# Kernel optimization log

Measured on AMD Instinct MI355X. Metric: run time of the kernel, lower is better.

## Reference

```python
import jax, jax.numpy as jnp
import numpy as np

PATCH = 16
B, C, H, W = 4, 3, 512, 512
N = 4096  # patches per image


def setup_inputs() -> dict:
    key = jax.random.key(0)
    k1, k2, k3, k4 = jax.random.split(key, 4)
    fuse = jax.random.normal(k1, (B, C, H, W), jnp.float32)
    img1 = jax.random.normal(k2, (B, C, H, W), jnp.float32)
    img2 = jax.random.normal(k3, (B, C, H, W), jnp.float32)
    # valid top-left (h, w) so h+PATCH <= H, w+PATCH <= W
    coords = jax.random.randint(k4, (B, N, 2), 0, H - PATCH + 1, dtype=jnp.int32)
    return {"fuse": fuse, "img1": img1, "img2": img2, "coords": coords}


def _extract_patches(image, coords):
    # image: [B,C,H,W], coords: [B,N,2] -> patches [B,C,N,P] with P=PATCH*PATCH
    c = image.shape[1]

    def one(img_b, hw):
        p = jax.lax.dynamic_slice(img_b, (0, hw[0], hw[1]), (c, PATCH, PATCH))
        return p.reshape(c, PATCH * PATCH)

    pat = jax.vmap(jax.vmap(one, in_axes=(None, 0)), in_axes=(0, 0))(image, coords)  # [B,N,C,P]
    return jnp.transpose(pat, (0, 2, 1, 3))  # [B,C,N,P]


def reference(fuse, img1, img2, coords):
    pf = _extract_patches(fuse, coords)
    p1 = _extract_patches(img1, coords)
    p2 = _extract_patches(img2, coords)
    mu1 = jnp.mean(p1, axis=-1, keepdims=True)
    mu2 = jnp.mean(p2, axis=-1, keepdims=True)
    sd1 = jnp.sqrt(jnp.mean((p1 - mu1) ** 2, axis=-1, keepdims=True))
    sd2 = jnp.sqrt(jnp.mean((p2 - mu2) ** 2, axis=-1, keepdims=True))
    denom = sd1 + sd2 + 1e-6
    target = (sd1 / denom) * p1 + (sd2 / denom) * p2
    return jnp.mean(jnp.abs(pf - target))
```

## Files before the change

kernel.cpp:

```cpp
#include <hip/hip_runtime.h>

#define BD 4
#define CD 3
#define HD 512
#define WD 512
#define NPAT 4096
#define NP (BD * NPAT)
#define PLANE (HD * WD)
#define PPW 2
#define PPB (PPW * 4)
#define NBLK (NP / PPB)
#define TOTAL_ELEMS (4.0 * 3.0 * 4096.0 * 256.0)

typedef float f4 __attribute__((ext_vector_type(4), aligned(4)));

template <int CTRL>
__device__ __forceinline__ float dpp_add(float x) {
    int y = __builtin_amdgcn_update_dpp(0, __float_as_int(x), CTRL, 0xF, 0xF, true);
    return x + __int_as_float(y);
}

__device__ __forceinline__ float wave_sum64(float x) {
    x = dpp_add<0xB1>(x);
    x = dpp_add<0x4E>(x);
    x = dpp_add<0x124>(x);
    x = dpp_add<0x128>(x);
    x += __shfl_xor(x, 16, 64);
    x += __shfl_xor(x, 32, 64);
    return x;
}

__global__ __launch_bounds__(256) void build_order(
    const int* __restrict__ coords, unsigned int* __restrict__ order)
{
    __shared__ unsigned short cnt[256][18];
    __shared__ unsigned short part[16][17];
    __shared__ unsigned int   base[16];

    const int t = threadIdx.x;
    const int b = blockIdx.x;
    const int key16 = t >> 4;
    const int sub   = t & 15;

    #pragma unroll
    for (int k = 0; k < 16; ++k) cnt[t][k] = 0;
    __syncthreads();

    const int2* c2 = (const int2*)coords;
    unsigned int pk[16];
    #pragma unroll
    for (int i = 0; i < 16; ++i) {
        const int p = (b << 12) + (i << 8) + t;
        const int2 hw = c2[p];
        pk[i] = ((unsigned)b << 18) | ((unsigned)hw.x << 9) | (unsigned)hw.y;
        cnt[t][hw.x >> 5]++;
    }
    __syncthreads();

    unsigned run = 0;
    #pragma unroll
    for (int tt = sub * 16; tt < sub * 16 + 16; ++tt) run += cnt[tt][key16];
    part[key16][sub] = (unsigned short)run;
    __syncthreads();

    if (t < 16) {
        unsigned r = 0;
        #pragma unroll
        for (int s = 0; s < 16; ++s) { unsigned v = part[t][s]; part[t][s] = (unsigned short)r; r += v; }
        base[t] = r;
    }
    __syncthreads();
    if (t == 0) {
        unsigned r = 0;
        #pragma unroll
        for (int k = 0; k < 16; ++k) { unsigned v = base[k]; base[k] = r; r += v; }
    }
    __syncthreads();

    {
        unsigned r = part[key16][sub];
        #pragma unroll
        for (int tt = sub * 16; tt < sub * 16 + 16; ++tt) {
            unsigned v = cnt[tt][key16]; cnt[tt][key16] = (unsigned short)r; r += v;
        }
    }
    __syncthreads();

    #pragma unroll
    for (int i = 0; i < 16; ++i) {
        const unsigned key = (pk[i] >> 14) & 15;
        const unsigned pos = base[key] + cnt[t][key];
        cnt[t][key]++;
        order[(b << 12) + pos] = pk[i];
    }
}

__global__ __launch_bounds__(256) void patch_stage1(
    const float* __restrict__ fuse,
    const float* __restrict__ img1,
    const float* __restrict__ img2,
    const unsigned int* __restrict__ order,
    float* __restrict__ partials)
{
    const int lane = threadIdx.x & 63;
    const int wave = threadIdx.x >> 6;
    const int bid  = blockIdx.x;
    const int slot0 = (((bid & 7) * (NBLK / 8) + (bid >> 3)) << 3) + wave * PPW;

    const uint2 ord = *(const uint2*)(order + slot0);

    const int wA = ord.x & 511, hA = (ord.x >> 9) & 511, bA = ord.x >> 18;
    const int wB = ord.y & 511, hB = (ord.y >> 9) & 511, bB = ord.y >> 18;

    const int roff = (lane >> 2) * WD + (lane & 3) * 4;
    const size_t baseA = ((size_t)(bA * CD) * HD + hA) * WD + wA + roff;
    const size_t baseB = ((size_t)(bB * CD) * HD + hB) * WD + wB + roff;

    f4 vfA[3], v1A[3], v2A[3], vfB[3], v1B[3], v2B[3];
    #pragma unroll
    for (int c = 0; c < CD; ++c) {
        vfA[c] = *(const f4*)(fuse + baseA + (size_t)c * PLANE);
        v1A[c] = *(const f4*)(img1 + baseA + (size_t)c * PLANE);
        v2A[c] = *(const f4*)(img2 + baseA + (size_t)c * PLANE);
        vfB[c] = *(const f4*)(fuse + baseB + (size_t)c * PLANE);
        v1B[c] = *(const f4*)(img1 + baseB + (size_t)c * PLANE);
        v2B[c] = *(const f4*)(img2 + baseB + (size_t)c * PLANE);
    }

    float s1[2][3], q1[2][3], s2[2][3], q2[2][3];
    #pragma unroll
    for (int c = 0; c < CD; ++c) {
        s1[0][c] = v1A[c].x + v1A[c].y + v1A[c].z + v1A[c].w;
        q1[0][c] = v1A[c].x*v1A[c].x + v1A[c].y*v1A[c].y + v1A[c].z*v1A[c].z + v1A[c].w*v1A[c].w;
        s2[0][c] = v2A[c].x + v2A[c].y + v2A[c].z + v2A[c].w;
        q2[0][c] = v2A[c].x*v2A[c].x + v2A[c].y*v2A[c].y + v2A[c].z*v2A[c].z + v2A[c].w*v2A[c].w;
        s1[1][c] = v1B[c].x + v1B[c].y + v1B[c].z + v1B[c].w;
        q1[1][c] = v1B[c].x*v1B[c].x + v1B[c].y*v1B[c].y + v1B[c].z*v1B[c].z + v1B[c].w*v1B[c].w;
        s2[1][c] = v2B[c].x + v2B[c].y + v2B[c].z + v2B[c].w;
        q2[1][c] = v2B[c].x*v2B[c].x + v2B[c].y*v2B[c].y + v2B[c].z*v2B[c].z + v2B[c].w*v2B[c].w;
    }

    #pragma unroll
    for (int u = 0; u < 2; ++u) {
        #pragma unroll
        for (int c = 0; c < CD; ++c) {
            s1[u][c] = wave_sum64(s1[u][c]);
            q1[u][c] = wave_sum64(q1[u][c]);
            s2[u][c] = wave_sum64(s2[u][c]);
            q2[u][c] = wave_sum64(q2[u][c]);
        }
    }

    const float inv = 1.f / 256.f;
    float acc = 0.f;
    #pragma unroll
    for (int u = 0; u < 2; ++u) {
        #pragma unroll
        for (int c = 0; c < CD; ++c) {
            const float mu1 = s1[u][c] * inv;
            const float mu2 = s2[u][c] * inv;
            const float sd1 = sqrtf(fmaxf(q1[u][c] * inv - mu1 * mu1, 0.f));
            const float sd2 = sqrtf(fmaxf(q2[u][c] * inv - mu2 * mu2, 0.f));
            const float denom = sd1 + sd2 + 1e-6f;
            const float w1 = sd1 / denom;
            const float w2 = sd2 / denom;
            const f4 vf = u ? vfB[c] : vfA[c];
            const f4 v1 = u ? v1B[c] : v1A[c];
            const f4 v2 = u ? v2B[c] : v2A[c];
            acc += fabsf(vf.x - (w1 * v1.x + w2 * v2.x))
                 + fabsf(vf.y - (w1 * v1.y + w2 * v2.y))
                 + fabsf(vf.z - (w1 * v1.z + w2 * v2.z))
                 + fabsf(vf.w - (w1 * v1.w + w2 * v2.w));
        }
    }

    acc = wave_sum64(acc);

    __shared__ float partsm[4];
    if (lane == 0) partsm[wave] = acc;
    __syncthreads();
    if (threadIdx.x == 0)
        partials[bid] = partsm[0] + partsm[1] + partsm[2] + partsm[3];
}

__global__ __launch_bounds__(256) void patch_stage2(
    const float* __restrict__ partials, float* __restrict__ out)
{
    float s = 0.f;
    for (int i = threadIdx.x; i < NBLK; i += 256)
        s += partials[i];

    s = wave_sum64(s);

    __shared__ float partsm[4];
    const int lane = threadIdx.x & 63;
    const int wave = threadIdx.x >> 6;
    if (lane == 0) partsm[wave] = s;
    __syncthreads();
    if (threadIdx.x == 0)
        out[0] = (partsm[0] + partsm[1] + partsm[2] + partsm[3]) * (float)(1.0 / TOTAL_ELEMS);
}

extern "C" void kernel_launch(void* const* d_in, const int* in_sizes, int n_in,
                              void* d_out, int out_size, void* d_ws, size_t ws_size,
                              hipStream_t stream) {
    const float* fuse   = (const float*)d_in[0];
    const float* img1   = (const float*)d_in[1];
    const float* img2   = (const float*)d_in[2];
    const int*   coords = (const int*)d_in[3];
    float* out = (float*)d_out;

    unsigned int* order    = (unsigned int*)d_ws;
    float*        partials = (float*)((char*)d_ws + NP * 4);

    build_order<<<BD, 256, 0, stream>>>(coords, order);
    patch_stage1<<<NBLK, 256, 0, stream>>>(fuse, img1, img2, order, partials);
    patch_stage2<<<1, 256, 0, stream>>>(partials, out);
}
```

Before: 30.73 us.

## Sort patches by 2D 32x32 tile buckets instead of row bands

The counting-sort key in build_order changes from 16 row bands to 256 spatial tiles (h/32, w/32). The goal is to make consecutive stage1 blocks read spatially nearby patches and improve L2/cache reuse. To support the larger key space, build_order now uses byte counters in a large padded LDS array, a per-thread serial column scan, and a wave shuffle prefix scan. In exchange, the sort kernel uses much more shared memory and does a longer serial scan.

```diff
diff --git a/kernel.cpp b/kernel.cpp
--- a/kernel.cpp
+++ b/kernel.cpp
@@ -11,6 +11,7 @@
 #define PPB (PPW * 4)
 #define NBLK (NP / PPB)
 #define TOTAL_ELEMS (4.0 * 3.0 * 4096.0 * 256.0)
+#define CSTRIDE 260
 
 typedef float f4 __attribute__((ext_vector_type(4), aligned(4)));
 
@@ -33,64 +34,67 @@
 __global__ __launch_bounds__(256) void build_order(
     const int* __restrict__ coords, unsigned int* __restrict__ order)
 {
-    __shared__ unsigned short cnt[256][18];
-    __shared__ unsigned short part[16][17];
-    __shared__ unsigned int   base[16];
+    __shared__ unsigned char  cnt[256 * CSTRIDE];
+    __shared__ unsigned short total[256];
+    __shared__ unsigned int   base[256];
 
     const int t = threadIdx.x;
     const int b = blockIdx.x;
-    const int key16 = t >> 4;
-    const int sub   = t & 15;
-
-    #pragma unroll
-    for (int k = 0; k < 16; ++k) cnt[t][k] = 0;
+
+    {
+        unsigned int* row = (unsigned int*)(cnt + t * CSTRIDE);
+        #pragma unroll
+        for (int k = 0; k < CSTRIDE / 4; ++k) row[k] = 0u;
+    }
     __syncthreads();
 
     const int2* c2 = (const int2*)coords;
-    unsigned int pk[16];
+    unsigned int  pk[16];
+    unsigned char kk[16];
     #pragma unroll
     for (int i = 0; i < 16; ++i) {
         const int p = (b << 12) + (i << 8) + t;
         const int2 hw = c2[p];
         pk[i] = ((unsigned)b << 18) | ((unsigned)hw.x << 9) | (unsigned)hw.y;
-        cnt[t][hw.x >> 5]++;
-    }
-    __syncthreads();
-
-    unsigned run = 0;
-    #pragma unroll
-    for (int tt = sub * 16; tt < sub * 16 + 16; ++tt) run += cnt[tt][key16];
-    part[key16][sub] = (unsigned short)run;
-    __syncthreads();
-
-    if (t < 16) {
-        unsigned r = 0;
-        #pragma unroll
-        for (int s = 0; s < 16; ++s) { unsigned v = part[t][s]; part[t][s] = (unsigned short)r; r += v; }
-        base[t] = r;
-    }
-    __syncthreads();
-    if (t == 0) {
-        unsigned r = 0;
-        #pragma unroll
-        for (int k = 0; k < 16; ++k) { unsigned v = base[k]; base[k] = r; r += v; }
+        kk[i] = (unsigned char)(((hw.x >> 5) << 4) | (hw.y >> 5));
+        cnt[t * CSTRIDE + kk[i]]++;
     }
     __syncthreads();
 
     {
-        unsigned r = part[key16][sub];
-        #pragma unroll
-        for (int tt = sub * 16; tt < sub * 16 + 16; ++tt) {
-            unsigned v = cnt[tt][key16]; cnt[tt][key16] = (unsigned short)r; r += v;
-        }
+        unsigned int run = 0;
+        for (int tt = 0; tt < 256; ++tt) {
+            const unsigned int v = cnt[tt * CSTRIDE + t];
+            cnt[tt * CSTRIDE + t] = (unsigned char)run;
+            run += v;
+        }
+        total[t] = (unsigned short)run;
+    }
+    __syncthreads();
+
+    if (t < 64) {
+        const unsigned int t0 = total[4 * t],     t1 = total[4 * t + 1];
+        const unsigned int t2 = total[4 * t + 2], t3 = total[4 * t + 3];
+        const unsigned int lsum = t0 + t1 + t2 + t3;
+        unsigned int x = lsum;
+        #pragma unroll
+        for (int d = 1; d < 64; d <<= 1) {
+            const unsigned int v = __shfl_up(x, d, 64);
+            if (t >= d) x += v;
+        }
+        const unsigned int excl = x - lsum;
+        base[4 * t]     = excl;
+        base[4 * t + 1] = excl + t0;
+        base[4 * t + 2] = excl + t0 + t1;
+        base[4 * t + 3] = excl + t0 + t1 + t2;
     }
     __syncthreads();
 
     #pragma unroll
     for (int i = 0; i < 16; ++i) {
-        const unsigned key = (pk[i] >> 14) & 15;
-        const unsigned pos = base[key] + cnt[t][key];
-        cnt[t][key]++;
+        const int key = kk[i];
+        const unsigned int pos = base[key] + cnt[t * CSTRIDE + key];
+        cnt[t * CSTRIDE + key]++;
         order[(b << 12) + pos] = pk[i];
     }
 }
```

After: 32.33 us. +5.2%, slower.
